# Kernel optimization log

Hardware: AMD Instinct MI355X
Metric: run time of the kernel (lower is better)

## Reference

```python
import jax, jax.numpy as jnp
import numpy as np

B, S, C = 256, 169, 512      # batch, input seq_len (hardcoded 169 in source), n_attn
H, TT, HS = 256, 256, 16     # n_head, ctx_len, head_size (all forced by hardcoded shapes)
OUT = 64                     # output Linear(16, 64)


def setup_inputs() -> dict:
    key = jax.random.key(0)
    ks = jax.random.split(key, 13)
    s_in = 1.0 / np.sqrt(C)
    s_hs = 1.0 / np.sqrt(HS)
    return {
        "x": jax.random.normal(ks[0], (B, S, C), dtype=jnp.float32),
        "time_w": jax.random.normal(ks[1], (H, TT), dtype=jnp.float32) * 0.1,
        "time_alpha": jax.random.normal(ks[2], (H, 1, TT), dtype=jnp.float32) * 0.1 + 1.0,
        "time_beta": jax.random.normal(ks[3], (H, TT, 1), dtype=jnp.float32) * 0.1 + 1.0,
        "time_gamma": jax.random.normal(ks[4], (TT, 1), dtype=jnp.float32) * 0.1 + 1.0,
        "key_w": jax.random.normal(ks[5], (HS, C), dtype=jnp.float32) * s_in,
        "key_b": jax.random.normal(ks[6], (HS,), dtype=jnp.float32) * s_in,
        "value_w": jax.random.normal(ks[7], (HS, C), dtype=jnp.float32) * s_in,
        "value_b": jax.random.normal(ks[8], (HS,), dtype=jnp.float32) * s_in,
        "recep_w": jax.random.normal(ks[9], (HS, C), dtype=jnp.float32) * s_in,
        "recep_b": jax.random.normal(ks[10], (HS,), dtype=jnp.float32) * s_in,
        "out_w": jax.random.normal(ks[11], (OUT, HS), dtype=jnp.float32) * s_hs,
        "out_b": jax.random.normal(ks[12], (OUT,), dtype=jnp.float32) * s_hs,
    }


def reference(x, time_w, time_alpha, time_beta, time_gamma,
              key_w, key_b, value_w, value_b, recep_w, recep_b,
              out_w, out_b):
    # --- build the time-decay matrix via the pad/tile shift trick ---
    w = jnp.pad(time_w, ((0, 0), (0, TT)))            # (H, 2TT)
    w = jnp.tile(w, (1, TT))                          # (H, 2TT*TT)
    w = w[:, :-TT].reshape(H, TT, 2 * TT - 1)
    w = w[:, :, TT - 1:]                              # (H, TT, TT)
    w = w * time_alpha * time_beta                    # (H, TT, TT)

    # --- channel-half time shift: first C/2 channels shifted back by 1 step ---
    half = C // 2
    shifted = jnp.pad(x[:, :, :half], ((0, 0), (1, 0), (0, 0)))[:, :-1]
    x = jnp.concatenate([shifted, x[:, :, half:]], axis=-1)

    # --- projections (torch Linear: y = x @ W.T + b) ---
    k = x @ key_w.T + key_b                           # (B, S, HS)
    v = x @ value_w.T + value_b
    r = x @ recep_w.T + recep_b

    pad_len = TT - S                                  # 256 - 169 = 87
    r = jnp.pad(r, ((0, 0), (0, pad_len), (0, 0)))    # (B, TT, HS)

    k = jnp.exp(jnp.clip(k, -60.0, 30.0))
    sum_k = jnp.cumsum(k, axis=1)                     # (B, S, HS)
    sum_k = jnp.pad(sum_k, ((0, 0), (0, pad_len), (0, 0)))  # (B, TT, HS)

    kv = k * v                                        # (B, S, HS)
    kv = jnp.pad(kv, ((0, 0), (0, pad_len), (0, 0)))  # (B, TT, HS)

    # einsum('htu,bhc->btc') == contract u first, then (t,h) matmul against kv's seq axis
    w2 = w.sum(axis=-1)                               # (H, TT): sum_u w[h,t,u]
    wkv = jnp.einsum('ht,bhc->btc', w2, kv)           # (B, TT, HS)

    # original divides by zero-padded sum_k in the padded tail; guard with 1 there
    denom = jnp.where(sum_k == 0, jnp.ones_like(sum_k), sum_k)
    rwkv = jax.nn.sigmoid(r) * wkv / denom            # (B, TT, HS)

    rwkv = rwkv @ out_w.T + out_b                     # (B, TT, 64)
    rwkv = rwkv * time_gamma[:TT]                     # (TT,1) broadcast
    return rwkv
```

## Files before the change

### kernel.cpp

```cpp
#include <hip/hip_runtime.h>

typedef unsigned short u16;
typedef unsigned int u32;
typedef __attribute__((ext_vector_type(8))) __bf16 bf16x8;
typedef __attribute__((ext_vector_type(4))) __bf16 bf16x4;
typedef __attribute__((ext_vector_type(4))) float f32x4;

#define S_LEN 169
#define SP 192

#define W2T_WS 0
#define WPK_WS 98304
#define KE_WS  147456
#define KV_WS  (KE_WS + 2883584)
#define SG_WS  (KV_WS + 1441792)

#define SKE  0
#define SKV  11264
#define SG2  16896
#define SKVT 28160
#define SRB  34304
#define SSS  54784
#define SOW  55808
#define S_LDS 60928

__global__ __launch_bounds__(1024) void k0_kernel(
    const float* __restrict__ time_w,
    const float* __restrict__ time_alpha,
    const float* __restrict__ time_beta,
    const float* __restrict__ key_w,
    const float* __restrict__ value_w,
    const float* __restrict__ recep_w,
    char* __restrict__ ws)
{
    __bf16* w2t = (__bf16*)(ws + W2T_WS);
    const int blk = blockIdx.x;
    if (blk >= 192) {
        const int m = blk - 192;
        const float* wmat = (m == 0) ? key_w : (m == 1) ? value_w : recep_w;
        const int g = threadIdx.x;
        if (g < 1024) {
            const float* src = wmat + g * 8;
            float4 f0 = *(const float4*)src;
            float4 f1 = *(const float4*)(src + 4);
            bf16x8 p;
            p[0]=(__bf16)f0.x; p[1]=(__bf16)f0.y; p[2]=(__bf16)f0.z; p[3]=(__bf16)f0.w;
            p[4]=(__bf16)f1.x; p[5]=(__bf16)f1.y; p[6]=(__bf16)f1.z; p[7]=(__bf16)f1.w;
            int hs = g >> 6, rem = g & 63, ks = rem >> 2, q = rem & 3;
            int fid = ks * 64 + q * 16 + hs;
            *(bf16x8*)(ws + WPK_WS + m * 16384 + fid * 16) = p;
        }
        return;
    }
    __shared__ float tw[256];
    __shared__ float al[256];
    __shared__ float part[4][256];
    const int s = blk;
    const int t = threadIdx.x & 255;
    const int p = threadIdx.x >> 8;
    if (s >= S_LEN) {
        if (p == 0) w2t[t * SP + s] = (__bf16)0.f;
        return;
    }
    if (p == 0) { tw[t] = time_w[s * 256 + t]; al[t] = time_alpha[s * 256 + t]; }
    __syncthreads();
    const int u0 = p << 6;
    const int u1 = (u0 + 64 < t + 1) ? (u0 + 64) : (t + 1);
    float acc = 0.f;
    for (int u = u0; u < u1; ++u)
        acc = fmaf(tw[255 + u - t], al[u], acc);
    part[p][t] = acc;
    __syncthreads();
    if (p == 0)
        w2t[t * SP + s] = (__bf16)(time_beta[s * 256 + t] *
                                   (part[0][t] + part[1][t] + part[2][t] + part[3][t]));
}

__global__ __launch_bounds__(192) void g_kernel(
    const float* __restrict__ x,
    const float* __restrict__ key_b,
    const float* __restrict__ value_b,
    const float* __restrict__ recep_b,
    char* __restrict__ ws)
{
    __shared__ __align__(16) char smem[17408];
    const int tid  = threadIdx.x;
    const int lane = tid & 63;
    const int wid  = tid >> 6;
    const int q    = lane >> 4;
    const int hs   = lane & 15;
    const int blk  = blockIdx.x;
    const int b    = blk / 11;
    const int slab = blk - b * 11;
    const int t0   = slab * 16;
    const float* xb = x + (size_t)b * (S_LEN * 512);

    bf16x8 bfrag[16];
    #pragma unroll
    for (int ks = 0; ks < 16; ++ks)
        bfrag[ks] = *(const bf16x8*)(ws + WPK_WS + wid * 16384 + (ks * 64 + lane) * 16);
    const float* bv = (wid == 0) ? key_b : (wid == 1) ? value_b : recep_b;
    const float bias = bv[hs];

    float4 st[12];
    int    sv[12];
    #pragma unroll
    for (int it = 0; it < 12; ++it) {
        int idx = tid + it * 192; if (idx > 2175) idx = 2175;
        int row = idx >> 7, c4 = idx & 127;
        int g   = t0 - 1 + row;
        sv[it]  = ((unsigned)g < (unsigned)S_LEN) ? 1 : 0;
        int gc  = g < 0 ? 0 : (g > S_LEN - 1 ? S_LEN - 1 : g);
        st[it]  = *(const float4*)(xb + (size_t)gc * 512 + c4 * 4);
    }
    #pragma unroll
    for (int it = 0; it < 12; ++it) {
        int idx = tid + it * 192; if (idx > 2175) idx = 2175;
        int row = idx >> 7, c4 = idx & 127;
        float4 f = st[it];
        if (!sv[it]) f = (float4){0.f, 0.f, 0.f, 0.f};
        bf16x4 p;
        p[0] = (__bf16)f.x; p[1] = (__bf16)f.y; p[2] = (__bf16)f.z; p[3] = (__bf16)f.w;
        u32 off = (u32)row * 1024 + ((((u32)c4) * 8u) ^ (((u32)(row & 7)) << 4));
        *(bf16x4*)(smem + off) = p;
    }
    __syncthreads();

    f32x4 acc = (f32x4){0.f, 0.f, 0.f, 0.f};
    #pragma unroll
    for (int ks = 0; ks < 16; ++ks) {
        int r = hs + ((ks < 8) ? 0 : 1);
        u32 off = (u32)r * 1024 + (((u32)(ks * 64 + q * 16)) ^ (((u32)(r & 7)) << 4));
        bf16x8 a = *(const bf16x8*)(smem + off);
        acc = __builtin_amdgcn_mfma_f32_16x16x32_bf16(a, bfrag[ks], acc, 0, 0, 0);
    }
    __syncthreads();

    float* raw = (float*)smem;
    #pragma unroll
    for (int rg = 0; rg < 4; ++rg)
        raw[wid * 256 + (q * 4 + rg) * 16 + hs] = acc[rg] + bias;
    __syncthreads();

    float* keg = (float*)(ws + KE_WS);
    __bf16* kvg = (__bf16*)(ws + KV_WS);
    float* sgg = (float*)(ws + SG_WS);
    for (int i = tid; i < 256; i += 192) {
        int tl = i >> 4, h = i & 15;
        int t  = t0 + tl;
        if (t < S_LEN) {
            float kk = fminf(fmaxf(raw[i], -60.f), 30.f);
            float ke = __expf(kk);
            size_t o = ((size_t)b * 176 + t) * 16 + h;
            keg[o] = ke;
            kvg[o] = (__bf16)(ke * raw[256 + i]);
            sgg[o] = 1.f / (1.f + __expf(-raw[512 + i]));
        }
    }
}

__global__ __launch_bounds__(256) void scan_kernel(
    const char* __restrict__ wsr,
    const float* __restrict__ out_w, const float* __restrict__ out_b,
    const float* __restrict__ gamma,
    float* __restrict__ out)
{
    __shared__ __align__(16) char smem[S_LDS];
    const int tid  = threadIdx.x;
    const int lane = tid & 63;
    const int wid  = tid >> 6;
    const int q    = lane >> 4;
    const int hs   = lane & 15;
    const int b    = blockIdx.x;
    const __bf16* w2t = (const __bf16*)(wsr + W2T_WS);
    const float4* keb = (const float4*)(wsr + KE_WS + (size_t)b * 11264);
    const float4* kvb = (const float4*)(wsr + KV_WS + (size_t)b * 5632);
    const float4* sgb = (const float4*)(wsr + SG_WS + (size_t)b * 11264);

    #pragma unroll
    for (int it = 0; it < 3; ++it) {
        int i = tid + (it << 8);
        if (i < 676) {
            ((float4*)(smem + SKE))[i] = keb[i];
            ((float4*)(smem + SG2))[i] = sgb[i];
        }
        if (i < 338) ((float4*)(smem + SKV))[i] = kvb[i];
    }
    for (int i = tid; i < 2560; i += 256) {
        int o = i / 40, c = i - o * 40;
        ((__bf16*)(smem + SOW))[i] = (c < 16) ? (__bf16)out_w[o * 16 + c] : (__bf16)0.f;
    }
    for (int i = tid; i < 4096; i += 256) {
        int row = i >> 4, c = 16 + (i & 15);
        ((__bf16*)(smem + SRB))[row * 40 + c] = (__bf16)0.f;
    }
    for (int i = tid; i < 368; i += 256) {
        int h2 = i & 15; int t = S_LEN + (i >> 4);
        u32 off = ((u32)(h2 * 384 + t * 2)) ^ (((u32)(h2 & 7)) << 4);
        *(__bf16*)(smem + SKVT + off) = (__bf16)0.f;
    }
    __syncthreads();

    float* KE = (float*)(smem + SKE);
    float* GG = (float*)(smem + SG2);
    float* SEG = (float*)(smem + SSS);
    const int h  = tid & 15;
    const int sg = tid >> 4;
    const int ts = sg * 11;
    const int te = (ts + 11 < S_LEN) ? ts + 11 : S_LEN;
    {
        float ssum = 0.f;
        for (int t = ts; t < te; ++t) ssum += KE[t * 16 + h];
        SEG[sg * 16 + h] = ssum;
    }
    __syncthreads();
    {
        float run = 0.f;
        for (int s2 = 0; s2 < sg; ++s2) run += SEG[s2 * 16 + h];
        for (int t = ts; t < te; ++t) {
            run += KE[t * 16 + h];
            u32 off = ((u32)(h * 384 + t * 2)) ^ (((u32)(h & 7)) << 4);
            *(__bf16*)(smem + SKVT + off) = ((const __bf16*)(smem + SKV))[t * 16 + h];
            GG[t * 16 + h] = GG[t * 16 + h] / run;
        }
    }
    __syncthreads();

    f32x4 wa[4];
    #pragma unroll
    for (int mi = 0; mi < 4; ++mi) wa[mi] = (f32x4){0.f,0.f,0.f,0.f};
    #pragma unroll
    for (int s0 = 0; s0 < SP; s0 += 32) {
        int scol = s0 + (q << 3);
        u32 boff = ((u32)(hs * 384 + scol * 2)) ^ (((u32)(hs & 7)) << 4);
        bf16x8 bfr = *(const bf16x8*)(smem + SKVT + boff);
        #pragma unroll
        for (int mi = 0; mi < 4; ++mi) {
            int row = (wid + (mi << 2)) * 16 + hs;
            bf16x8 afr = *(const bf16x8*)(w2t + row * SP + scol);
            wa[mi] = __builtin_amdgcn_mfma_f32_16x16x32_bf16(afr, bfr, wa[mi], 0,0,0);
        }
    }
    #pragma unroll
    for (int mi = 0; mi < 4; ++mi) {
        int tb = (wid + (mi << 2)) * 16 + (q << 2);
        #pragma unroll
        for (int rg = 0; rg < 4; ++rg) {
            int t = tb + rg;
            float fac = (t < S_LEN) ? GG[t * 16 + hs] : 0.5f;
            ((__bf16*)(smem + SRB))[t * 40 + hs] = (__bf16)(wa[mi][rg] * fac);
        }
    }
    __syncthreads();

    float obv[4];
    #pragma unroll
    for (int nt = 0; nt < 4; ++nt) obv[nt] = out_b[nt * 16 + hs];
    #pragma unroll
    for (int mi = 0; mi < 4; ++mi) {
        int mt = wid + (mi << 2);
        int arow = mt * 16 + hs;
        bf16x8 afr = *(const bf16x8*)(smem + SRB + (u32)(arow * 80 + (q << 4)));
        float gm[4];
        #pragma unroll
        for (int rg = 0; rg < 4; ++rg) gm[rg] = gamma[mt * 16 + (q << 2) + rg];
        #pragma unroll
        for (int nt = 0; nt < 4; ++nt) {
            int orow = nt * 16 + hs;
            bf16x8 bfr = *(const bf16x8*)(smem + SOW + (u32)(orow * 80 + (q << 4)));
            f32x4 zc = (f32x4){0.f,0.f,0.f,0.f};
            f32x4 d = __builtin_amdgcn_mfma_f32_16x16x32_bf16(afr, bfr, zc, 0,0,0);
            #pragma unroll
            for (int rg = 0; rg < 4; ++rg) {
                int t = mt * 16 + (q << 2) + rg;
                out[(size_t)b * 16384 + (size_t)t * 64 + nt * 16 + hs] = (d[rg] + obv[nt]) * gm[rg];
            }
        }
    }
}

extern "C" void kernel_launch(void* const* d_in, const int* in_sizes, int n_in,
                              void* d_out, int out_size, void* d_ws, size_t ws_size,
                              hipStream_t stream) {
    const float* x          = (const float*)d_in[0];
    const float* time_w     = (const float*)d_in[1];
    const float* time_alpha = (const float*)d_in[2];
    const float* time_beta  = (const float*)d_in[3];
    const float* time_gamma = (const float*)d_in[4];
    const float* key_w      = (const float*)d_in[5];
    const float* key_b      = (const float*)d_in[6];
    const float* value_w    = (const float*)d_in[7];
    const float* value_b    = (const float*)d_in[8];
    const float* recep_w    = (const float*)d_in[9];
    const float* recep_b    = (const float*)d_in[10];
    const float* out_w      = (const float*)d_in[11];
    const float* out_b      = (const float*)d_in[12];
    char* ws = (char*)d_ws;

    k0_kernel<<<195, 1024, 0, stream>>>(time_w, time_alpha, time_beta,
                                        key_w, value_w, recep_w, ws);
    g_kernel<<<2816, 192, 0, stream>>>(x, key_b, value_b, recep_b, ws);
    scan_kernel<<<256, 256, 0, stream>>>(ws, out_w, out_b, time_gamma, (float*)d_out);
}
```

Baseline: 41.89 us.

## Pre-pack decay matrix into MFMA fragment layout and store KE/sigmoid as bf16

The decay-matrix precompute now writes w2 directly in per-lane MFMA A-fragment order, so the scan kernel reads each fragment as one contiguous 16-byte load per lane instead of strided row reads. The exp(k) and sigmoid(r) intermediates are stored in bf16 instead of fp32, halving their workspace traffic and LDS staging. The scan stores reciprocal denominators separately and combines them with sigmoid at the output step. Running the cumulative sum over bf16-rounded exp(k) values adds precision loss.

```diff
diff --git a/kernel.cpp b/kernel.cpp
--- a/kernel.cpp
+++ b/kernel.cpp
@@ -9,15 +9,16 @@
 #define S_LEN 169
 #define SP 192
 
-#define W2T_WS 0
+#define W2A_WS 0
 #define WPK_WS 98304
 #define KE_WS  147456
-#define KV_WS  (KE_WS + 2883584)
+#define KV_WS  (KE_WS + 1441792)
 #define SG_WS  (KV_WS + 1441792)
 
 #define SKE  0
-#define SKV  11264
-#define SG2  16896
+#define SKV  5632
+#define SG2  11264
+#define DEN  16896
 #define SKVT 28160
 #define SRB  34304
 #define SSS  54784
@@ -33,23 +34,20 @@
     const float* __restrict__ recep_w,
     char* __restrict__ ws)
 {
-    __bf16* w2t = (__bf16*)(ws + W2T_WS);
     const int blk = blockIdx.x;
     if (blk >= 192) {
         const int m = blk - 192;
         const float* wmat = (m == 0) ? key_w : (m == 1) ? value_w : recep_w;
         const int g = threadIdx.x;
-        if (g < 1024) {
-            const float* src = wmat + g * 8;
-            float4 f0 = *(const float4*)src;
-            float4 f1 = *(const float4*)(src + 4);
-            bf16x8 p;
-            p[0]=(__bf16)f0.x; p[1]=(__bf16)f0.y; p[2]=(__bf16)f0.z; p[3]=(__bf16)f0.w;
-            p[4]=(__bf16)f1.x; p[5]=(__bf16)f1.y; p[6]=(__bf16)f1.z; p[7]=(__bf16)f1.w;
-            int hs = g >> 6, rem = g & 63, ks = rem >> 2, q = rem & 3;
-            int fid = ks * 64 + q * 16 + hs;
-            *(bf16x8*)(ws + WPK_WS + m * 16384 + fid * 16) = p;
-        }
+        const float* src = wmat + g * 8;
+        float4 f0 = *(const float4*)src;
+        float4 f1 = *(const float4*)(src + 4);
+        bf16x8 p;
+        p[0]=(__bf16)f0.x; p[1]=(__bf16)f0.y; p[2]=(__bf16)f0.z; p[3]=(__bf16)f0.w;
+        p[4]=(__bf16)f1.x; p[5]=(__bf16)f1.y; p[6]=(__bf16)f1.z; p[7]=(__bf16)f1.w;
+        int hs = g >> 6, rem = g & 63, ks = rem >> 2, q = rem & 3;
+        int fid = ks * 64 + q * 16 + hs;
+        *(bf16x8*)(ws + WPK_WS + m * 16384 + fid * 16) = p;
         return;
     }
     __shared__ float tw[256];
@@ -58,8 +56,10 @@
     const int s = blk;
     const int t = threadIdx.x & 255;
     const int p = threadIdx.x >> 8;
+    const u32 adr = (u32)((( (t >> 4) * 6 + (s >> 5)) * 64 + ((s >> 3) & 3) * 16 + (t & 15)) * 16
+                          + (s & 7) * 2);
     if (s >= S_LEN) {
-        if (p == 0) w2t[t * SP + s] = (__bf16)0.f;
+        if (p == 0) *(u16*)(ws + W2A_WS + adr) = 0;
         return;
     }
     if (p == 0) { tw[t] = time_w[s * 256 + t]; al[t] = time_alpha[s * 256 + t]; }
@@ -71,9 +71,11 @@
         acc = fmaf(tw[255 + u - t], al[u], acc);
     part[p][t] = acc;
     __syncthreads();
-    if (p == 0)
-        w2t[t * SP + s] = (__bf16)(time_beta[s * 256 + t] *
-                                   (part[0][t] + part[1][t] + part[2][t] + part[3][t]));
+    if (p == 0) {
+        __bf16 v = (__bf16)(time_beta[s * 256 + t] *
+                            (part[0][t] + part[1][t] + part[2][t] + part[3][t]));
+        *(u16*)(ws + W2A_WS + adr) = *(u16*)&v;
+    }
 }
 
 __global__ __launch_bounds__(192) void g_kernel(
@@ -142,9 +144,9 @@
         raw[wid * 256 + (q * 4 + rg) * 16 + hs] = acc[rg] + bias;
     __syncthreads();
 
-    float* keg = (float*)(ws + KE_WS);
+    __bf16* keg = (__bf16*)(ws + KE_WS);
     __bf16* kvg = (__bf16*)(ws + KV_WS);
-    float* sgg = (float*)(ws + SG_WS);
+    __bf16* sgg = (__bf16*)(ws + SG_WS);
     for (int i = tid; i < 256; i += 192) {
         int tl = i >> 4, h = i & 15;
         int t  = t0 + tl;
@@ -152,9 +154,9 @@
             float kk = fminf(fmaxf(raw[i], -60.f), 30.f);
             float ke = __expf(kk);
             size_t o = ((size_t)b * 176 + t) * 16 + h;
-            keg[o] = ke;
+            keg[o] = (__bf16)ke;
             kvg[o] = (__bf16)(ke * raw[256 + i]);
-            sgg[o] = 1.f / (1.f + __expf(-raw[512 + i]));
+            sgg[o] = (__bf16)(1.f / (1.f + __expf(-raw[512 + i])));
         }
     }
 }
@@ -172,19 +174,18 @@
     const int q    = lane >> 4;
     const int hs   = lane & 15;
     const int b    = blockIdx.x;
-    const __bf16* w2t = (const __bf16*)(wsr + W2T_WS);
-    const float4* keb = (const float4*)(wsr + KE_WS + (size_t)b * 11264);
+    const float4* keb = (const float4*)(wsr + KE_WS + (size_t)b * 5632);
     const float4* kvb = (const float4*)(wsr + KV_WS + (size_t)b * 5632);
-    const float4* sgb = (const float4*)(wsr + SG_WS + (size_t)b * 11264);
-
-    #pragma unroll
-    for (int it = 0; it < 3; ++it) {
+    const float4* sgb = (const float4*)(wsr + SG_WS + (size_t)b * 5632);
+
+    #pragma unroll
+    for (int it = 0; it < 2; ++it) {
         int i = tid + (it << 8);
-        if (i < 676) {
+        if (i < 338) {
             ((float4*)(smem + SKE))[i] = keb[i];
+            ((float4*)(smem + SKV))[i] = kvb[i];
             ((float4*)(smem + SG2))[i] = sgb[i];
         }
-        if (i < 338) ((float4*)(smem + SKV))[i] = kvb[i];
     }
     for (int i = tid; i < 2560; i += 256) {
         int o = i / 40, c = i - o * 40;
@@ -201,8 +202,9 @@
     }
     __syncthreads();
 
-    float* KE = (float*)(smem + SKE);
-    float* GG = (float*)(smem + SG2);
+    const __bf16* KE = (const __bf16*)(smem + SKE);
+    const __bf16* SGb = (const __bf16*)(smem + SG2);
+    float* DENi = (float*)(smem + DEN);
     float* SEG = (float*)(smem + SSS);
     const int h  = tid & 15;
     const int sg = tid >> 4;
@@ -210,7 +212,7 @@
     const int te = (ts + 11 < S_LEN) ? ts + 11 : S_LEN;
     {
         float ssum = 0.f;
-        for (int t = ts; t < te; ++t) ssum += KE[t * 16 + h];
+        for (int t = ts; t < te; ++t) ssum += (float)KE[t * 16 + h];
         SEG[sg * 16 + h] = ssum;
     }
     __syncthreads();
@@ -218,10 +220,10 @@
         float run = 0.f;
         for (int s2 = 0; s2 < sg; ++s2) run += SEG[s2 * 16 + h];
         for (int t = ts; t < te; ++t) {
-            run += KE[t * 16 + h];
+            run += (float)KE[t * 16 + h];
+            DENi[t * 16 + h] = 1.f / run;
             u32 off = ((u32)(h * 384 + t * 2)) ^ (((u32)(h & 7)) << 4);
-            *(__bf16*)(smem + SKVT + off) = ((const __bf16*)(smem + SKV))[t * 16 + h];
-            GG[t * 16 + h] = GG[t * 16 + h] / run;
+            *(u16*)(smem + SKVT + off) = ((const u16*)(smem + SKV))[t * 16 + h];
         }
     }
     __syncthreads();
@@ -230,14 +232,14 @@
     #pragma unroll
     for (int mi = 0; mi < 4; ++mi) wa[mi] = (f32x4){0.f,0.f,0.f,0.f};
     #pragma unroll
-    for (int s0 = 0; s0 < SP; s0 += 32) {
-        int scol = s0 + (q << 3);
+    for (int ks = 0; ks < 6; ++ks) {
+        int scol = ks * 32 + (q << 3);
         u32 boff = ((u32)(hs * 384 + scol * 2)) ^ (((u32)(hs & 7)) << 4);
         bf16x8 bfr = *(const bf16x8*)(smem + SKVT + boff);
         #pragma unroll
         for (int mi = 0; mi < 4; ++mi) {
-            int row = (wid + (mi << 2)) * 16 + hs;
-            bf16x8 afr = *(const bf16x8*)(w2t + row * SP + scol);
+            int rt = wid + (mi << 2);
+            bf16x8 afr = *(const bf16x8*)(wsr + W2A_WS + (u32)(((rt * 6 + ks) * 64 + lane) * 16));
             wa[mi] = __builtin_amdgcn_mfma_f32_16x16x32_bf16(afr, bfr, wa[mi], 0,0,0);
         }
     }
@@ -247,7 +249,7 @@
         #pragma unroll
         for (int rg = 0; rg < 4; ++rg) {
             int t = tb + rg;
-            float fac = (t < S_LEN) ? GG[t * 16 + hs] : 0.5f;
+            float fac = (t < S_LEN) ? (float)SGb[t * 16 + hs] * DENi[t * 16 + hs] : 0.5f;
             ((__bf16*)(smem + SRB))[t * 40 + hs] = (__bf16)(wa[mi][rg] * fac);
         }
     }
```

New measurement: 40.75 us. 1.03x faster.
